# Kernel tuning notes

Hardware: AMD Instinct MI355X
Metric: run time of the kernel (lower is better)

## Reference

```python
import jax, jax.numpy as jnp
import numpy as np

B, C_IN, C_OUT, H, W = 16, 256, 256, 64, 64
RANK, ORDER = 16, 2
EPS = 1e-5


def setup_inputs() -> dict:
    key = jax.random.key(0)
    k1, k2, k3 = jax.random.split(key, 3)
    x = jax.random.normal(k1, (B, C_IN, H, W), dtype=jnp.float32)
    # torch init: w_core ~ N(0, 1/(C_in*rank)), w_out ~ N(0, 1/rank)
    w_core = jax.random.normal(k2, (RANK, C_IN, RANK), dtype=jnp.float32) * (1.0 / (C_IN * RANK))
    w_out = jax.random.normal(k3, (RANK, C_OUT, RANK), dtype=jnp.float32) * (1.0 / RANK)
    return {"x": x, "w_core": w_core, "w_out": w_out}


def reference(x, w_core, w_out):
    # Per-pixel tensor-ring 1x1 conv.
    # Original chain for order=2 (share_core):
    #   T = einsum('achw,rck->arhwk', x, w_core)
    #   out = einsum('aebcf,afbcg,gdh->aedbch', T, T, w_out)
    #   y   = einsum('arohwr->aohw', out)   # ring trace over e==h
    # Equivalent: M[a,h,w] is rank x rank; P = M^order; y_d = tr(P @ W_d)
    M = jnp.einsum('achw,rck->ahwrk', x, w_core)  # [B,H,W,r,r]
    P = M
    for _ in range(ORDER - 1):
        P = jnp.einsum('ahwef,ahwfg->ahweg', P, M)
    y = jnp.einsum('ahweg,gde->adhw', P, w_out)  # [B,C_out,H,W]
    # InstanceNorm2d (affine=False, biased variance) + Softsign
    mean = jnp.mean(y, axis=(2, 3), keepdims=True)
    var = jnp.var(y, axis=(2, 3), keepdims=True)
    yn = (y - mean) * jax.lax.rsqrt(var + EPS)
    return yn / (1.0 + jnp.abs(yn))
```

## Files before the change

### kernel.cpp

```cpp
#include <hip/hip_runtime.h>

#define HW 4096
#define NC 256
#define ND 256
#define NB 16

typedef _Float16 half4_t __attribute__((ext_vector_type(4)));
typedef _Float16 half8_t __attribute__((ext_vector_type(8)));
typedef float floatx2 __attribute__((ext_vector_type(2)));
typedef float floatx4 __attribute__((ext_vector_type(4)));

#define MSCALE 64.0f
#define INV_MSCALE2 (1.0f / 4096.0f)
#define EPS_SCALED (1e-5f * 4096.0f * 4096.0f)

__global__ __launch_bounds__(256) void prep_weights(
        const float* __restrict__ w_core, const float* __restrict__ w_out,
        _Float16* __restrict__ W1p, _Float16* __restrict__ W2p) {
    int tid = blockIdx.x * 256 + threadIdx.x;
    int l   = tid & 63;
    int rt  = (tid >> 6) & 15;
    int ks  = (tid >> 10) & 7;
    int sel = tid >> 13;
    int row = l & 15, kg = l >> 4;
    half8_t v;
    if (sel == 0) {
        int r = rt, k = row;
#pragma unroll
        for (int j = 0; j < 8; ++j) {
            int c = ks * 32 + kg * 8 + j;
            v[j] = (_Float16)(w_core[r * 4096 + c * 16 + k] * MSCALE);
        }
        *(half8_t*)&W1p[(size_t)((ks * 16 + rt) * 64 + l) * 8] = v;
    } else {
        int d = rt * 16 + row;
#pragma unroll
        for (int j = 0; j < 8; ++j) {
            int eg = ks * 32 + kg * 8 + j, e = eg >> 4, g = eg & 15;
            v[j] = (_Float16)w_out[g * 4096 + d * 16 + e];
        }
        *(half8_t*)&W2p[(size_t)((ks * 16 + rt) * 64 + l) * 8] = v;
    }
}

template<bool F16Y>
__global__ __launch_bounds__(256, 2) void compute_y(
        const float* __restrict__ x, const _Float16* __restrict__ W1p,
        const _Float16* __restrict__ W2p, float* __restrict__ y,
        _Float16* __restrict__ y16, float* __restrict__ ssum,
        float* __restrict__ ssq) {
    __shared__ __align__(16) _Float16 R1[16384];
    __shared__ __align__(16) _Float16 R2[16384];

    const int t = threadIdx.x;
    const int l = t & 63, w = t >> 6;
    const int a = blockIdx.x >> 6;
    const int pixbase = (blockIdx.x & 63) * 64;
    const int row16 = l & 15, kg = l >> 4;
    const float* xa = x + (size_t)a * NC * HW + pixbase;

    {
        const int px = t & 63;
        const int o0 = t >> 6;
#pragma unroll
        for (int q = 0; q < 8; ++q) {
            const int oct = q * 4 + o0;
            half8_t hv;
#pragma unroll
            for (int j = 0; j < 8; ++j)
                hv[j] = (_Float16)xa[(size_t)(oct * 8 + j) * HW + px];
            *(half8_t*)&R1[px * 256 + ((oct ^ (px & 15)) << 3)] = hv;
        }
    }
    __syncthreads();

    floatx4 acc[4][4];
#pragma unroll
    for (int i = 0; i < 4; ++i)
#pragma unroll
        for (int j = 0; j < 4; ++j) acc[i][j] = (floatx4){0.f, 0.f, 0.f, 0.f};
    {
        const half8_t* W1v = (const half8_t*)W1p;
        for (int ks = 0; ks < 8; ++ks) {
            half8_t af[4];
#pragma unroll
            for (int rq = 0; rq < 4; ++rq)
                af[rq] = W1v[(ks * 16 + w * 4 + rq) * 64 + l];
#pragma unroll
            for (int pt = 0; pt < 4; ++pt) {
                const int px = pt * 16 + row16;
                half8_t bf = *(const half8_t*)
                    &R1[px * 256 + (((ks * 4 + kg) ^ row16) << 3)];
#pragma unroll
                for (int rq = 0; rq < 4; ++rq)
                    acc[rq][pt] = __builtin_amdgcn_mfma_f32_16x16x32_f16(
                                      af[rq], bf, acc[rq][pt], 0, 0, 0);
            }
        }
    }
#pragma unroll
    for (int rq = 0; rq < 4; ++rq) {
        const int rk4 = (w * 4 + rq) * 4 + kg;
#pragma unroll
        for (int pt = 0; pt < 4; ++pt) {
            const int px = pt * 16 + row16;
            half4_t hv;
#pragma unroll
            for (int r2 = 0; r2 < 4; ++r2) hv[r2] = (_Float16)acc[rq][pt][r2];
            *(half4_t*)&R2[px * 256 + ((rk4 ^ row16) << 2)] = hv;
        }
    }
    __syncthreads();

    {
        const int p = t >> 2, qe = t & 3, ps = p & 15;
        const _Float16* Mp = &R2[p * 256];
        float Af[4][16];
#pragma unroll
        for (int i = 0; i < 4; ++i) {
            const int e = i * 4 + qe;
#pragma unroll
            for (int f4 = 0; f4 < 4; ++f4) {
                half4_t v = *(const half4_t*)
                    &Mp[(((e * 4 + f4) ^ ps) << 2)];
#pragma unroll
                for (int j = 0; j < 4; ++j) Af[i][f4 * 4 + j] = (float)v[j];
            }
        }
        floatx2 Pacc[4][8];
#pragma unroll
        for (int i = 0; i < 4; ++i)
#pragma unroll
            for (int g2 = 0; g2 < 8; ++g2) Pacc[i][g2] = (floatx2){0.f, 0.f};
#pragma unroll
        for (int f = 0; f < 16; ++f) {
            floatx2 Bg[8];
#pragma unroll
            for (int g4 = 0; g4 < 4; ++g4) {
                half4_t v = *(const half4_t*)
                    &Mp[(((f * 4 + g4) ^ ps) << 2)];
                Bg[g4 * 2]     = (floatx2){(float)v[0], (float)v[1]};
                Bg[g4 * 2 + 1] = (floatx2){(float)v[2], (float)v[3]};
            }
#pragma unroll
            for (int i = 0; i < 4; ++i) {
                floatx2 a2 = {Af[i][f], Af[i][f]};
#pragma unroll
                for (int g2 = 0; g2 < 8; ++g2)
                    Pacc[i][g2] = __builtin_elementwise_fma(a2, Bg[g2], Pacc[i][g2]);
            }
        }
#pragma unroll
        for (int i = 0; i < 4; ++i) {
            const int e = i * 4 + qe;
#pragma unroll
            for (int h2 = 0; h2 < 2; ++h2) {
                half8_t hv;
#pragma unroll
                for (int j = 0; j < 8; ++j)
                    hv[j] = (_Float16)Pacc[i][h2 * 4 + (j >> 1)][j & 1];
                *(half8_t*)&R1[p * 256 + (((e * 2 + h2) ^ ps) << 3)] = hv;
            }
        }
    }
    __syncthreads();

    half8_t pb[8];
#pragma unroll
    for (int ks = 0; ks < 8; ++ks)
        pb[ks] = *(const half8_t*)
            &R1[(w * 16 + row16) * 256 + (((ks * 4 + kg) ^ row16) << 3)];

    floatx4 cacc[4][4];
#pragma unroll
    for (int i = 0; i < 4; ++i)
#pragma unroll
        for (int j = 0; j < 4; ++j) cacc[i][j] = (floatx4){0.f, 0.f, 0.f, 0.f};
    {
        const half8_t* W2v = (const half8_t*)W2p;
        for (int ks = 0; ks < 8; ++ks) {
            half8_t af[4];
#pragma unroll
            for (int dq = 0; dq < 4; ++dq)
                af[dq] = W2v[(ks * 16 + w * 4 + dq) * 64 + l];
#pragma unroll
            for (int pt = 0; pt < 4; ++pt) {
                const int px = pt * 16 + row16;
                half8_t bf = *(const half8_t*)
                    &R1[px * 256 + (((ks * 4 + kg) ^ row16) << 3)];
#pragma unroll
                for (int dq = 0; dq < 4; ++dq)
                    cacc[dq][pt] = __builtin_amdgcn_mfma_f32_16x16x32_f16(
                                       af[dq], bf, cacc[dq][pt], 0, 0, 0);
            }
        }
    }

    float*     ya   = y   + (size_t)a * ND * HW + pixbase;
    _Float16*  ya16 = F16Y ? (y16 + (size_t)a * ND * HW + pixbase) : nullptr;
#pragma unroll
    for (int dq = 0; dq < 4; ++dq) {
        const int dbase = (w * 4 + dq) * 16 + kg * 4;
#pragma unroll
        for (int r2 = 0; r2 < 4; ++r2) {
            const int d = dbase + r2;
            float s = 0.f, q2 = 0.f;
#pragma unroll
            for (int pt = 0; pt < 4; ++pt) {
                float v;
                if (F16Y) {
                    _Float16 hv = (_Float16)cacc[dq][pt][r2];
                    ya16[(size_t)d * HW + pt * 16 + row16] = hv;
                    v = (float)hv;
                } else {
                    v = cacc[dq][pt][r2] * INV_MSCALE2;
                    ya[(size_t)d * HW + pt * 16 + row16] = v;
                }
                s += v; q2 += v * v;
            }
#pragma unroll
            for (int off = 1; off < 16; off <<= 1) {
                s  += __shfl_xor(s, off);
                q2 += __shfl_xor(q2, off);
            }
            if (row16 == 0) {
                atomicAdd(&ssum[a * 256 + d], s);
                atomicAdd(&ssq [a * 256 + d], q2);
            }
        }
    }
}

__global__ __launch_bounds__(256) void stats_finalize(
        const float* __restrict__ ssum, const float* __restrict__ ssq,
        float* __restrict__ mean_o, float* __restrict__ istd_o, float eps) {
    int i = blockIdx.x * 256 + threadIdx.x;
    float m = ssum[i] * (1.f / HW);
    float v = ssq[i] * (1.f / HW) - m * m;
    mean_o[i] = m;
    istd_o[i] = rsqrtf(v + eps);
}

__global__ __launch_bounds__(256) void finalize_f16(
        const _Float16* __restrict__ y16, const float* __restrict__ mean_a,
        const float* __restrict__ istd_a, float* __restrict__ out) {
    const size_t base = ((size_t)blockIdx.x * 256 + threadIdx.x) * 16;
    const int ad = (int)(base >> 12);
    const float m = mean_a[ad], s = istd_a[ad];
    half8_t h0 = *(const half8_t*)&y16[base];
    half8_t h1 = *(const half8_t*)&y16[base + 8];
    float o[16];
#pragma unroll
    for (int j = 0; j < 8; ++j) {
        float z0 = ((float)h0[j] - m) * s;
        float z1 = ((float)h1[j] - m) * s;
        o[j]     = z0 / (1.f + fabsf(z0));
        o[8 + j] = z1 / (1.f + fabsf(z1));
    }
#pragma unroll
    for (int q = 0; q < 4; ++q)
        *(float4*)&out[base + q * 4] =
            make_float4(o[q * 4], o[q * 4 + 1], o[q * 4 + 2], o[q * 4 + 3]);
}

__global__ __launch_bounds__(256) void finalize_f32(
        float* __restrict__ y, const float* __restrict__ mean_a,
        const float* __restrict__ istd_a) {
    const int i4 = blockIdx.x * 256 + threadIdx.x;
    const int ad = i4 >> 10;
    const float m = mean_a[ad], s = istd_a[ad];
    float4 v = ((const float4*)y)[i4];
    float vv[4] = {v.x, v.y, v.z, v.w};
#pragma unroll
    for (int lq = 0; lq < 4; ++lq) {
        float z = (vv[lq] - m) * s;
        vv[lq] = z / (1.f + fabsf(z));
    }
    ((float4*)y)[i4] = make_float4(vv[0], vv[1], vv[2], vv[3]);
}

extern "C" void kernel_launch(void* const* d_in, const int* in_sizes, int n_in,
                              void* d_out, int out_size, void* d_ws, size_t ws_size,
                              hipStream_t stream) {
    const float* x      = (const float*)d_in[0];
    const float* w_core = (const float*)d_in[1];
    const float* w_out  = (const float*)d_in[2];
    float* y = (float*)d_out;

    char* wsb = (char*)d_ws;
    _Float16* W1p = (_Float16*)wsb;
    _Float16* W2p = (_Float16*)(wsb + 131072);
    float* ssum   = (float*)(wsb + 262144);
    float* ssq    = (float*)(wsb + 278528);
    float* mean_a = (float*)(wsb + 294912);
    float* istd_a = (float*)(wsb + 311296);
    _Float16* y16 = (_Float16*)(wsb + 327680);

    const size_t need_f16 = 327680 + (size_t)NB * ND * HW * sizeof(_Float16);
    const bool use_f16 = ws_size >= need_f16;

    hipMemsetAsync(ssum, 0, 2 * 4096 * sizeof(float), stream);
    prep_weights<<<64, 256, 0, stream>>>(w_core, w_out, W1p, W2p);
    if (use_f16) {
        compute_y<true><<<1024, 256, 0, stream>>>(x, W1p, W2p, y, y16, ssum, ssq);
        stats_finalize<<<16, 256, 0, stream>>>(ssum, ssq, mean_a, istd_a, EPS_SCALED);
        finalize_f16<<<4096, 256, 0, stream>>>(y16, mean_a, istd_a, y);
    } else {
        compute_y<false><<<1024, 256, 0, stream>>>(x, W1p, W2p, y, nullptr, ssum, ssq);
        stats_finalize<<<16, 256, 0, stream>>>(ssum, ssq, mean_a, istd_a, 1e-5f);
        finalize_f32<<<16384, 256, 0, stream>>>(y, mean_a, istd_a);
    }
}
```

Baseline: 86.32 us.

## Halve pixel tile, raise occupancy, prefetch weights, fold stats and memset kernels

Each compute block now handles 32 pixels instead of 64, which halves shared memory and accumulator registers so launch bounds can target 4 blocks per SM with twice as many blocks. Weight fragments are software-prefetched one k-step ahead in both MFMA GEMMs, and the second GEMM's weights are loaded early, before the M^2 stage. The separate memset and stats_finalize launches are removed: prep_weights zeroes the accumulators and the finalize kernels compute mean and inverse std inline. Smaller tiles mean more redundant weight loads per pixel and more atomic traffic, in exchange for better latency hiding and fewer launches.

```diff
diff --git a/kernel.cpp b/kernel.cpp
--- a/kernel.cpp
+++ b/kernel.cpp
@@ -16,8 +16,10 @@
 
 __global__ __launch_bounds__(256) void prep_weights(
         const float* __restrict__ w_core, const float* __restrict__ w_out,
-        _Float16* __restrict__ W1p, _Float16* __restrict__ W2p) {
+        _Float16* __restrict__ W1p, _Float16* __restrict__ W2p,
+        float* __restrict__ ssum) {
     int tid = blockIdx.x * 256 + threadIdx.x;
+    if (tid < 8192) ssum[tid] = 0.f;
     int l   = tid & 63;
     int rt  = (tid >> 6) & 15;
     int ks  = (tid >> 10) & 7;
@@ -44,27 +46,27 @@
 }
 
 template<bool F16Y>
-__global__ __launch_bounds__(256, 2) void compute_y(
+__global__ __launch_bounds__(256, 4) void compute_y(
         const float* __restrict__ x, const _Float16* __restrict__ W1p,
         const _Float16* __restrict__ W2p, float* __restrict__ y,
         _Float16* __restrict__ y16, float* __restrict__ ssum,
         float* __restrict__ ssq) {
-    __shared__ __align__(16) _Float16 R1[16384];
-    __shared__ __align__(16) _Float16 R2[16384];
+    __shared__ __align__(16) _Float16 R1[8192];
+    __shared__ __align__(16) _Float16 R2[8192];
 
     const int t = threadIdx.x;
     const int l = t & 63, w = t >> 6;
-    const int a = blockIdx.x >> 6;
-    const int pixbase = (blockIdx.x & 63) * 64;
+    const int a = blockIdx.x >> 7;
+    const int pixbase = (blockIdx.x & 127) * 32;
     const int row16 = l & 15, kg = l >> 4;
     const float* xa = x + (size_t)a * NC * HW + pixbase;
 
     {
-        const int px = t & 63;
-        const int o0 = t >> 6;
-#pragma unroll
-        for (int q = 0; q < 8; ++q) {
-            const int oct = q * 4 + o0;
+        const int px = t & 31;
+        const int o0 = t >> 5;
+#pragma unroll
+        for (int q = 0; q < 4; ++q) {
+            const int oct = q * 8 + o0;
             half8_t hv;
 #pragma unroll
             for (int j = 0; j < 8; ++j)
@@ -74,20 +76,24 @@
     }
     __syncthreads();
 
-    floatx4 acc[4][4];
+    floatx4 acc[4][2];
 #pragma unroll
     for (int i = 0; i < 4; ++i)
 #pragma unroll
-        for (int j = 0; j < 4; ++j) acc[i][j] = (floatx4){0.f, 0.f, 0.f, 0.f};
+        for (int j = 0; j < 2; ++j) acc[i][j] = (floatx4){0.f, 0.f, 0.f, 0.f};
     {
         const half8_t* W1v = (const half8_t*)W1p;
+        half8_t af[4], afn[4];
+#pragma unroll
+        for (int rq = 0; rq < 4; ++rq) af[rq] = W1v[(w * 4 + rq) * 64 + l];
         for (int ks = 0; ks < 8; ++ks) {
-            half8_t af[4];
-#pragma unroll
-            for (int rq = 0; rq < 4; ++rq)
-                af[rq] = W1v[(ks * 16 + w * 4 + rq) * 64 + l];
-#pragma unroll
-            for (int pt = 0; pt < 4; ++pt) {
+            if (ks < 7) {
+#pragma unroll
+                for (int rq = 0; rq < 4; ++rq)
+                    afn[rq] = W1v[((ks + 1) * 16 + w * 4 + rq) * 64 + l];
+            }
+#pragma unroll
+            for (int pt = 0; pt < 2; ++pt) {
                 const int px = pt * 16 + row16;
                 half8_t bf = *(const half8_t*)
                     &R1[px * 256 + (((ks * 4 + kg) ^ row16) << 3)];
@@ -96,13 +102,15 @@
                     acc[rq][pt] = __builtin_amdgcn_mfma_f32_16x16x32_f16(
                                       af[rq], bf, acc[rq][pt], 0, 0, 0);
             }
+#pragma unroll
+            for (int rq = 0; rq < 4; ++rq) af[rq] = afn[rq];
         }
     }
 #pragma unroll
     for (int rq = 0; rq < 4; ++rq) {
         const int rk4 = (w * 4 + rq) * 4 + kg;
 #pragma unroll
-        for (int pt = 0; pt < 4; ++pt) {
+        for (int pt = 0; pt < 2; ++pt) {
             const int px = pt * 16 + row16;
             half4_t hv;
 #pragma unroll
@@ -112,13 +120,18 @@
     }
     __syncthreads();
 
+    const half8_t* W2v = (const half8_t*)W2p;
+    half8_t caf[4], cafn[4];
+#pragma unroll
+    for (int dq = 0; dq < 4; ++dq) caf[dq] = W2v[(w * 4 + dq) * 64 + l];
+
     {
-        const int p = t >> 2, qe = t & 3, ps = p & 15;
+        const int p = t >> 3, qe = t & 7, ps = p & 15;
         const _Float16* Mp = &R2[p * 256];
-        float Af[4][16];
-#pragma unroll
-        for (int i = 0; i < 4; ++i) {
-            const int e = i * 4 + qe;
+        float Af[2][16];
+#pragma unroll
+        for (int i = 0; i < 2; ++i) {
+            const int e = i * 8 + qe;
 #pragma unroll
             for (int f4 = 0; f4 < 4; ++f4) {
                 half4_t v = *(const half4_t*)
@@ -127,9 +140,9 @@
                 for (int j = 0; j < 4; ++j) Af[i][f4 * 4 + j] = (float)v[j];
             }
         }
-        floatx2 Pacc[4][8];
-#pragma unroll
-        for (int i = 0; i < 4; ++i)
+        floatx2 Pacc[2][8];
+#pragma unroll
+        for (int i = 0; i < 2; ++i)
 #pragma unroll
             for (int g2 = 0; g2 < 8; ++g2) Pacc[i][g2] = (floatx2){0.f, 0.f};
 #pragma unroll
@@ -143,7 +156,7 @@
                 Bg[g4 * 2 + 1] = (floatx2){(float)v[2], (float)v[3]};
             }
 #pragma unroll
-            for (int i = 0; i < 4; ++i) {
+            for (int i = 0; i < 2; ++i) {
                 floatx2 a2 = {Af[i][f], Af[i][f]};
 #pragma unroll
                 for (int g2 = 0; g2 < 8; ++g2)
@@ -151,8 +164,8 @@
             }
         }
 #pragma unroll
-        for (int i = 0; i < 4; ++i) {
-            const int e = i * 4 + qe;
+        for (int i = 0; i < 2; ++i) {
+            const int e = i * 8 + qe;
 #pragma unroll
             for (int h2 = 0; h2 < 2; ++h2) {
                 half8_t hv;
@@ -165,35 +178,29 @@
     }
     __syncthreads();
 
-    half8_t pb[8];
-#pragma unroll
-    for (int ks = 0; ks < 8; ++ks)
-        pb[ks] = *(const half8_t*)
-            &R1[(w * 16 + row16) * 256 + (((ks * 4 + kg) ^ row16) << 3)];
-
-    floatx4 cacc[4][4];
+    floatx4 cacc[4][2];
 #pragma unroll
     for (int i = 0; i < 4; ++i)
 #pragma unroll
-        for (int j = 0; j < 4; ++j) cacc[i][j] = (floatx4){0.f, 0.f, 0.f, 0.f};
-    {
-        const half8_t* W2v = (const half8_t*)W2p;
-        for (int ks = 0; ks < 8; ++ks) {
-            half8_t af[4];
+        for (int j = 0; j < 2; ++j) cacc[i][j] = (floatx4){0.f, 0.f, 0.f, 0.f};
+    for (int ks = 0; ks < 8; ++ks) {
+        if (ks < 7) {
 #pragma unroll
             for (int dq = 0; dq < 4; ++dq)
-                af[dq] = W2v[(ks * 16 + w * 4 + dq) * 64 + l];
-#pragma unroll
-            for (int pt = 0; pt < 4; ++pt) {
-                const int px = pt * 16 + row16;
-                half8_t bf = *(const half8_t*)
-                    &R1[px * 256 + (((ks * 4 + kg) ^ row16) << 3)];
-#pragma unroll
-                for (int dq = 0; dq < 4; ++dq)
-                    cacc[dq][pt] = __builtin_amdgcn_mfma_f32_16x16x32_f16(
-                                       af[dq], bf, cacc[dq][pt], 0, 0, 0);
-            }
-        }
+                cafn[dq] = W2v[((ks + 1) * 16 + w * 4 + dq) * 64 + l];
+        }
+#pragma unroll
+        for (int pt = 0; pt < 2; ++pt) {
+            const int px = pt * 16 + row16;
+            half8_t bf = *(const half8_t*)
+                &R1[px * 256 + (((ks * 4 + kg) ^ row16) << 3)];
+#pragma unroll
+            for (int dq = 0; dq < 4; ++dq)
+                cacc[dq][pt] = __builtin_amdgcn_mfma_f32_16x16x32_f16(
+                                   caf[dq], bf, cacc[dq][pt], 0, 0, 0);
+        }
+#pragma unroll
+        for (int dq = 0; dq < 4; ++dq) caf[dq] = cafn[dq];
     }
 
     float*     ya   = y   + (size_t)a * ND * HW + pixbase;
@@ -206,7 +213,7 @@
             const int d = dbase + r2;
             float s = 0.f, q2 = 0.f;
 #pragma unroll
-            for (int pt = 0; pt < 4; ++pt) {
+            for (int pt = 0; pt < 2; ++pt) {
                 float v;
                 if (F16Y) {
                     _Float16 hv = (_Float16)cacc[dq][pt][r2];
@@ -231,22 +238,14 @@
     }
 }
 
-__global__ __launch_bounds__(256) void stats_finalize(
-        const float* __restrict__ ssum, const float* __restrict__ ssq,
-        float* __restrict__ mean_o, float* __restrict__ istd_o, float eps) {
-    int i = blockIdx.x * 256 + threadIdx.x;
-    float m = ssum[i] * (1.f / HW);
-    float v = ssq[i] * (1.f / HW) - m * m;
-    mean_o[i] = m;
-    istd_o[i] = rsqrtf(v + eps);
-}
-
 __global__ __launch_bounds__(256) void finalize_f16(
-        const _Float16* __restrict__ y16, const float* __restrict__ mean_a,
-        const float* __restrict__ istd_a, float* __restrict__ out) {
-    const size_t base = ((size_t)blockIdx.x * 256 + threadIdx.x) * 16;
-    const int ad = (int)(base >> 12);
-    const float m = mean_a[ad], s = istd_a[ad];
+        const _Float16* __restrict__ y16, const float* __restrict__ ssum,
+        const float* __restrict__ ssq, float* __restrict__ out) {
+    const int ad = blockIdx.x;
+    const float m  = ssum[ad] * (1.f / HW);
+    const float sv = ssq[ad] * (1.f / HW) - m * m;
+    const float s  = rsqrtf(sv + EPS_SCALED);
+    const size_t base = (size_t)ad * HW + threadIdx.x * 16;
     half8_t h0 = *(const half8_t*)&y16[base];
     half8_t h1 = *(const half8_t*)&y16[base + 8];
     float o[16];
@@ -264,11 +263,13 @@
 }
 
 __global__ __launch_bounds__(256) void finalize_f32(
-        float* __restrict__ y, const float* __restrict__ mean_a,
-        const float* __restrict__ istd_a) {
+        float* __restrict__ y, const float* __restrict__ ssum,
+        const float* __restrict__ ssq) {
     const int i4 = blockIdx.x * 256 + threadIdx.x;
     const int ad = i4 >> 10;
-    const float m = mean_a[ad], s = istd_a[ad];
+    const float m  = ssum[ad] * (1.f / HW);
+    const float sv = ssq[ad] * (1.f / HW) - m * m;
+    const float s  = rsqrtf(sv + 1e-5f);
     float4 v = ((const float4*)y)[i4];
     float vv[4] = {v.x, v.y, v.z, v.w};
 #pragma unroll
@@ -292,22 +293,17 @@
     _Float16* W2p = (_Float16*)(wsb + 131072);
     float* ssum   = (float*)(wsb + 262144);
     float* ssq    = (float*)(wsb + 278528);
-    float* mean_a = (float*)(wsb + 294912);
-    float* istd_a = (float*)(wsb + 311296);
-    _Float16* y16 = (_Float16*)(wsb + 327680);
-
-    const size_t need_f16 = 327680 + (size_t)NB * ND * HW * sizeof(_Float16);
+    _Float16* y16 = (_Float16*)(wsb + 294912);
+
+    const size_t need_f16 = 294912 + (size_t)NB * ND * HW * sizeof(_Float16);
     const bool use_f16 = ws_size >= need_f16;
 
-    hipMemsetAsync(ssum, 0, 2 * 4096 * sizeof(float), stream);
-    prep_weights<<<64, 256, 0, stream>>>(w_core, w_out, W1p, W2p);
+    prep_weights<<<64, 256, 0, stream>>>(w_core, w_out, W1p, W2p, ssum);
     if (use_f16) {
-        compute_y<true><<<1024, 256, 0, stream>>>(x, W1p, W2p, y, y16, ssum, ssq);
-        stats_finalize<<<16, 256, 0, stream>>>(ssum, ssq, mean_a, istd_a, EPS_SCALED);
-        finalize_f16<<<4096, 256, 0, stream>>>(y16, mean_a, istd_a, y);
+        compute_y<true><<<2048, 256, 0, stream>>>(x, W1p, W2p, y, y16, ssum, ssq);
+        finalize_f16<<<4096, 256, 0, stream>>>(y16, ssum, ssq, y);
     } else {
-        compute_y<false><<<1024, 256, 0, stream>>>(x, W1p, W2p, y, nullptr, ssum, ssq);
-        stats_finalize<<<16, 256, 0, stream>>>(ssum, ssq, mean_a, istd_a, 1e-5f);
-        finalize_f32<<<16384, 256, 0, stream>>>(y, mean_a, istd_a);
-    }
-}
+        compute_y<false><<<2048, 256, 0, stream>>>(x, W1p, W2p, y, nullptr, ssum, ssq);
+        finalize_f32<<<16384, 256, 0, stream>>>(y, ssum, ssq);
+    }
+}
```

Result: slower. 100.7 us (+16.7%).
